# Performance work log

Measured on AMD Instinct MI355X. Metric: run time of the kernel, lower is better.

Reference implementation:

```python
import jax, jax.numpy as jnp
import numpy as np

N_NODES = 50000
N_EDGES = 800000
NEG_SLOPE = 0.2  # PyG GATConv default


def _gat_layer(x, src, dst, n, W, a_src, a_dst, b, concat):
    """One GATConv layer (PyG semantics, eval mode so attention dropout is off).

    x: [N, F_in], src/dst: [E'] (self loops included), W: [F_in, H*C],
    a_src/a_dst: [H, C], b: [H*C] if concat else [C].
    """
    H, C = a_src.shape
    h = (x @ W).reshape(n, H, C)                      # [N, H, C]
    al_s = jnp.sum(h * a_src, axis=-1)                # [N, H]
    al_d = jnp.sum(h * a_dst, axis=-1)                # [N, H]
    e = jax.nn.leaky_relu(al_s[src] + al_d[dst], NEG_SLOPE)  # [E', H]
    # numerically stable softmax over incoming edges of each dst node
    m = jax.lax.stop_gradient(jax.ops.segment_max(e, dst, num_segments=n))
    m = jnp.where(jnp.isfinite(m), m, 0.0)
    ex = jnp.exp(e - m[dst])                          # [E', H]
    denom = jax.ops.segment_sum(ex, dst, num_segments=n)     # [N, H]
    alpha = ex / denom[dst]                           # safe: self loops => denom > 0
    out = jax.ops.segment_sum(alpha[:, :, None] * h[src], dst, num_segments=n)  # [N,H,C]
    out = out.reshape(n, H * C) if concat else out.mean(axis=1)
    return out + b


def setup_inputs() -> dict:
    key = jax.random.key(0)
    ks = jax.random.split(key, 8)
    in_dim, hid, heads, out_dim = 256, 32, 8, 16
    x = jax.random.normal(ks[0], (N_NODES, in_dim), dtype=jnp.float32)
    edge_index = jax.random.randint(ks[1], (2, N_EDGES), 0, N_NODES, dtype=jnp.int64)
    s1 = 1.0 / np.sqrt(in_dim)
    s2 = 1.0 / np.sqrt(heads * hid)
    return {
        "x": x,
        "edge_index": edge_index,
        "W1": jax.random.normal(ks[2], (in_dim, heads * hid), dtype=jnp.float32) * s1,
        "a_src1": jax.random.normal(ks[3], (heads, hid), dtype=jnp.float32) * s2,
        "a_dst1": jax.random.normal(ks[4], (heads, hid), dtype=jnp.float32) * s2,
        "b1": jnp.zeros((heads * hid,), dtype=jnp.float32),
        "W2": jax.random.normal(ks[5], (heads * hid, out_dim), dtype=jnp.float32) * s2,
        "a_src2": jax.random.normal(ks[6], (1, out_dim), dtype=jnp.float32) * 0.25,
        "a_dst2": jax.random.normal(ks[7], (1, out_dim), dtype=jnp.float32) * 0.25,
        "b2": jnp.zeros((out_dim,), dtype=jnp.float32),
    }


def reference(x, edge_index, W1, a_src1, a_dst1, b1, W2, a_src2, a_dst2, b2):
    n = x.shape[0]
    loops = jnp.arange(n, dtype=edge_index.dtype)
    src = jnp.concatenate([edge_index[0], loops])  # add_self_loops (PyG default)
    dst = jnp.concatenate([edge_index[1], loops])
    h = jax.nn.relu(_gat_layer(x, src, dst, n, W1, a_src1, a_dst1, b1, concat=True))
    # F.dropout(p=0.5, training=False) -> identity in eval mode
    h = _gat_layer(h, src, dst, n, W2, a_src2, a_dst2, b2, concat=False)
    return jax.nn.log_softmax(h, axis=1)
```

## Files before the change

kernel.cpp:

```cpp
#include <hip/hip_runtime.h>
#include <hip/hip_bf16.h>


#define LRELU(x) ((x) > 0.f ? (x) : 0.2f * (x))

typedef __attribute__((ext_vector_type(8))) short short8;
typedef __attribute__((ext_vector_type(8))) unsigned short ushort8;
typedef __attribute__((ext_vector_type(4))) float f32x4;

__device__ inline unsigned short f2b(float f) {
    __hip_bfloat16 h = __float2bfloat16(f);
    return *reinterpret_cast<unsigned short*>(&h);
}
__device__ inline float b2f(unsigned short u) {
    __hip_bfloat16 h;
    *reinterpret_cast<unsigned short*>(&h) = u;
    return __bfloat162float(h);
}


__global__ void k_init_deg(int* deg, int n) {
    int i = blockIdx.x * blockDim.x + threadIdx.x;
    if (i < n) deg[i] = 1;
}

__global__ void k_hist(const int* __restrict__ dst, int* deg, int E) {
    int i = blockIdx.x * blockDim.x + threadIdx.x;
    if (i < E) atomicAdd(&deg[dst[i]], 1);
}


__global__ __launch_bounds__(256) void k_scanA(const int* __restrict__ deg,
                                               int* __restrict__ tmp,
                                               int* __restrict__ blocksum, int n) {
    __shared__ int sc[256];
    int b = blockIdx.x, t = threadIdx.x;
    int i = b * 256 + t;
    int v = (i < n) ? deg[i] : 0;
    sc[t] = v;
    __syncthreads();
    for (int off = 1; off < 256; off <<= 1) {
        int x = 0;
        if (t >= off) x = sc[t - off];
        __syncthreads();
        sc[t] += x;
        __syncthreads();
    }
    if (i < n) tmp[i] = sc[t] - v;
    if (t == 255) blocksum[b] = sc[255];
}

__global__ __launch_bounds__(256) void k_scanB(const int* __restrict__ blocksum,
                                               int* __restrict__ blockpre, int nb) {
    __shared__ int sc[256];
    int t = threadIdx.x;
    int v = (t < nb) ? blocksum[t] : 0;
    sc[t] = v;
    __syncthreads();
    for (int off = 1; off < 256; off <<= 1) {
        int x = 0;
        if (t >= off) x = sc[t - off];
        __syncthreads();
        sc[t] += x;
        __syncthreads();
    }
    if (t < nb) blockpre[t] = sc[t] - v;
}

__global__ __launch_bounds__(256) void k_scanC(const int* __restrict__ tmp,
                                               const int* __restrict__ blockpre,
                                               int* __restrict__ offs,
                                               int* __restrict__ cursor, int n, int P) {
    int b = blockIdx.x, t = threadIdx.x;
    int i = b * 256 + t;
    if (i < n) {
        int o = tmp[i] + blockpre[b];
        offs[i] = o;
        cursor[i] = o;
    }
    if (i == 0) offs[n] = P;
}

__global__ void k_scatter(const int* __restrict__ src, const int* __restrict__ dst,
                          int* cursor, int* __restrict__ csr, int* __restrict__ dstv,
                          int E, int n) {
    int i = blockIdx.x * blockDim.x + threadIdx.x;
    int s, d;
    if (i < E) {
        s = src[i];
        d = dst[i];
    } else if (i < E + n) {
        s = i - E;
        d = s;
    } else {
        return;
    }
    int p = atomicAdd(&cursor[d], 1);
    csr[p] = s;
    dstv[p] = d;
}


__global__ __launch_bounds__(256) void k_prepw(const float* __restrict__ W,
                                               unsigned short* __restrict__ Wt) {
    int k = blockIdx.x;
    int nn = threadIdx.x;
    Wt[nn * 256 + k] = f2b(W[k * 256 + nn]);
}


__global__ __launch_bounds__(256) void k_gemm1(const float* __restrict__ A,
                                               const unsigned short* __restrict__ Wt,
                                               unsigned short* __restrict__ h1b, int M) {
    __shared__ unsigned short As[128][40];
    __shared__ unsigned short Bs[128][40];
    int t = threadIdx.x;
    int r0 = blockIdx.x * 128, c0 = blockIdx.y * 128;
    int srow = t >> 1, shalf = t & 1;
    int lane = t & 63, w = t >> 6;
    int lane15 = lane & 15, quad = lane >> 4;
    int rbw = (w & 1) * 64, cbw = (w >> 1) * 64;

    f32x4 acc[4][4];
#pragma unroll
    for (int i = 0; i < 4; i++)
#pragma unroll
        for (int j = 0; j < 4; j++) acc[i][j] = (f32x4)0.f;

    for (int k0 = 0; k0 < 256; k0 += 32) {
        {
            int row = r0 + srow;
            ushort8 p0, p1;
            if (row < M) {
                const float4* sp = (const float4*)&A[(size_t)row * 256 + k0 + shalf * 16];
                float4 f0 = sp[0], f1 = sp[1], f2 = sp[2], f3 = sp[3];
                p0[0] = f2b(f0.x); p0[1] = f2b(f0.y); p0[2] = f2b(f0.z); p0[3] = f2b(f0.w);
                p0[4] = f2b(f1.x); p0[5] = f2b(f1.y); p0[6] = f2b(f1.z); p0[7] = f2b(f1.w);
                p1[0] = f2b(f2.x); p1[1] = f2b(f2.y); p1[2] = f2b(f2.z); p1[3] = f2b(f2.w);
                p1[4] = f2b(f3.x); p1[5] = f2b(f3.y); p1[6] = f2b(f3.z); p1[7] = f2b(f3.w);
            } else {
                p0 = (ushort8)0; p1 = (ushort8)0;
            }
            *(ushort8*)&As[srow][shalf * 16] = p0;
            *(ushort8*)&As[srow][shalf * 16 + 8] = p1;
            const ushort8* bp = (const ushort8*)&Wt[(size_t)(c0 + srow) * 256 + k0 + shalf * 16];
            *(ushort8*)&Bs[srow][shalf * 16] = bp[0];
            *(ushort8*)&Bs[srow][shalf * 16 + 8] = bp[1];
        }
        __syncthreads();
        short8 af[4], bf[4];
#pragma unroll
        for (int i = 0; i < 4; i++)
            af[i] = *(const short8*)&As[rbw + i * 16 + lane15][quad * 8];
#pragma unroll
        for (int j = 0; j < 4; j++)
            bf[j] = *(const short8*)&Bs[cbw + j * 16 + lane15][quad * 8];
#pragma unroll
        for (int i = 0; i < 4; i++)
#pragma unroll
            for (int j = 0; j < 4; j++)
                acc[i][j] = __builtin_amdgcn_mfma_f32_16x16x32_bf16(af[i], bf[j], acc[i][j], 0, 0, 0);
        __syncthreads();
    }
#pragma unroll
    for (int i = 0; i < 4; i++) {
        int rowb = r0 + rbw + i * 16 + quad * 4;
#pragma unroll
        for (int j = 0; j < 4; j++) {
            int col = c0 + cbw + j * 16 + lane15;
#pragma unroll
            for (int r = 0; r < 4; r++) {
                int row = rowb + r;
                if (row < M) h1b[(size_t)row * 256 + col] = f2b(acc[i][j][r]);
            }
        }
    }
}


__global__ __launch_bounds__(256) void k_al1(const unsigned short* __restrict__ h1b,
                                             const float* __restrict__ asrc,
                                             const float* __restrict__ adst,
                                             float* __restrict__ als,
                                             float* __restrict__ ald) {
    int v = blockIdx.x, t = threadIdx.x;
    float hv = b2f(h1b[(size_t)v * 256 + t]);
    float ps = hv * asrc[t], pd = hv * adst[t];
#pragma unroll
    for (int off = 16; off; off >>= 1) {
        ps += __shfl_down(ps, off, 32);
        pd += __shfl_down(pd, off, 32);
    }
    if ((t & 31) == 0) {
        int h = t >> 5;
        als[v * 8 + h] = ps;
        ald[v * 8 + h] = pd;
    }
}


__global__ void k_w1(const int* __restrict__ csr, const int* __restrict__ dstv,
                     const float* __restrict__ als, const float* __restrict__ ald,
                     float* __restrict__ w, int P) {
    int i = blockIdx.x * blockDim.x + threadIdx.x;
    if (i >= P * 8) return;
    int p = i >> 3, h = i & 7;
    int u = csr[p], d = dstv[p];
    float x = als[u * 8 + h] + ald[d * 8 + h];
    w[i] = __expf(LRELU(x));
}

__global__ void k_w2(const int* __restrict__ csr, const int* __restrict__ dstv,
                     const float* __restrict__ als, const float* __restrict__ ald,
                     float* __restrict__ w, int P) {
    int p = blockIdx.x * blockDim.x + threadIdx.x;
    if (p >= P) return;
    float x = als[csr[p]] + ald[dstv[p]];
    w[p] = __expf(LRELU(x));
}


__global__ __launch_bounds__(128) void k_agg1(const int* __restrict__ csr,
                                              const int* __restrict__ offs,
                                              const float* __restrict__ w1,
                                              const unsigned short* __restrict__ h1b,
                                              const float* __restrict__ b1,
                                              unsigned short* __restrict__ x2b) {
    int v = blockIdx.x;
    int t = threadIdx.x;
    int start = offs[v];
    int deg = offs[v + 1] - start;
    __shared__ int su[32];
    __shared__ float ws[256];
    int h = t >> 4;
    float a0 = 0.f, a1 = 0.f, wsum = 0.f;
    for (int base = 0; base < deg; base += 32) {
        int cnt = min(32, deg - base);
        if (base) __syncthreads();
        if (t < cnt) su[t] = csr[start + base + t];
        for (int i = t; i < cnt * 8; i += 128) ws[i] = w1[(size_t)(start + base) * 8 + i];
        __syncthreads();
        for (int e = 0; e < cnt; e++) {
            float wv = ws[e * 8 + h];
            const unsigned int* hp = (const unsigned int*)(h1b + (size_t)su[e] * 256);
            unsigned int pk = hp[t];
            float f0 = b2f((unsigned short)(pk & 0xffffu));
            float f1 = b2f((unsigned short)(pk >> 16));
            a0 += wv * f0;
            a1 += wv * f1;
            wsum += wv;
        }
    }
    const float2* b1v = (const float2*)b1;
    float2 bb = b1v[t];
    float inv = 1.0f / wsum;
    float o0 = a0 * inv + bb.x;
    float o1 = a1 * inv + bb.y;
    o0 = o0 > 0.f ? o0 : 0.f;
    o1 = o1 > 0.f ? o1 : 0.f;
    unsigned int opk = (unsigned int)f2b(o0) | ((unsigned int)f2b(o1) << 16);
    ((unsigned int*)(x2b + (size_t)v * 256))[t] = opk;
}


__global__ __launch_bounds__(256) void k_gemm2(const unsigned short* __restrict__ Xb,
                                               const float* __restrict__ W,
                                               const float* __restrict__ asrc,
                                               const float* __restrict__ adst,
                                               float* __restrict__ h2,
                                               float* __restrict__ als,
                                               float* __restrict__ ald, int n) {
    __shared__ float xs[16][260];
    __shared__ float ws[256 * 16];
    int t = threadIdx.x;
    int r0 = blockIdx.x * 16;
#pragma unroll
    for (int i = 0; i < 16; i++) ws[t + i * 256] = W[t + i * 256];
#pragma unroll
    for (int i = 0; i < 16; i++) {
        int row = r0 + i;
        xs[i][t] = (row < n) ? b2f(Xb[(size_t)row * 256 + t]) : 0.f;
    }
    __syncthreads();
    int nl = t >> 4, j = t & 15;
    float acc = 0.f;
    const float4* xv = (const float4*)&xs[nl][0];
#pragma unroll 8
    for (int k4 = 0; k4 < 64; k4++) {
        float4 a = xv[k4];
        int k = k4 * 4;
        acc += a.x * ws[k * 16 + j] + a.y * ws[(k + 1) * 16 + j] +
               a.z * ws[(k + 2) * 16 + j] + a.w * ws[(k + 3) * 16 + j];
    }
    int row = r0 + nl;
    float ps = acc * asrc[j], pd = acc * adst[j];
#pragma unroll
    for (int off = 8; off; off >>= 1) {
        ps += __shfl_down(ps, off, 16);
        pd += __shfl_down(pd, off, 16);
    }
    if (row < n) {
        h2[row * 16 + j] = acc;
        if (j == 0) {
            als[row] = ps;
            ald[row] = pd;
        }
    }
}


__global__ __launch_bounds__(256) void k_agg2(const int* __restrict__ csr,
                                              const int* __restrict__ offs,
                                              const float* __restrict__ w2,
                                              const float* __restrict__ h2,
                                              const float* __restrict__ b2,
                                              float* __restrict__ out, int n) {
    int v = blockIdx.x * 4 + (threadIdx.x >> 6);
    if (v >= n) return;
    int lane = threadIdx.x & 63;
    int start = offs[v];
    int deg = offs[v + 1] - start;
    int c = lane & 15, q = lane >> 4;
    float acc = 0.f, wsum = 0.f;
    for (int e = q; e < deg; e += 4) {
        int p = start + e;
        float wv = w2[p];
        int u = csr[p];
        acc += wv * h2[(size_t)u * 16 + c];
        wsum += wv;
    }
    acc += __shfl_xor(acc, 32, 64);
    acc += __shfl_xor(acc, 16, 64);
    wsum += __shfl_xor(wsum, 32, 64);
    wsum += __shfl_xor(wsum, 16, 64);
    float o = acc / wsum + b2[c];
    float mx = o;
#pragma unroll
    for (int off = 8; off; off >>= 1) mx = fmaxf(mx, __shfl_xor(mx, off, 16));
    float s = __expf(o - mx);
#pragma unroll
    for (int off = 8; off; off >>= 1) s += __shfl_xor(s, off, 16);
    float res = o - mx - __logf(s);
    if (q == 0) out[(size_t)v * 16 + c] = res;
}


extern "C" void kernel_launch(void* const* d_in, const int* in_sizes, int n_in,
                              void* d_out, int out_size, void* d_ws, size_t ws_size,
                              hipStream_t stream) {
    const float* x = (const float*)d_in[0];
    const int* ei = (const int*)d_in[1];
    const float* W1 = (const float*)d_in[2];
    const float* asrc1 = (const float*)d_in[3];
    const float* adst1 = (const float*)d_in[4];
    const float* b1 = (const float*)d_in[5];
    const float* W2 = (const float*)d_in[6];
    const float* asrc2 = (const float*)d_in[7];
    const float* adst2 = (const float*)d_in[8];
    const float* b2 = (const float*)d_in[9];
    float* out = (float*)d_out;

    int n = in_sizes[0] / 256;
    int E = in_sizes[1] / 2;
    int P = E + n;
    const int* src = ei;
    const int* dst = ei + E;
    int NB = (n + 255) / 256;

    char* p = (char*)d_ws;
    auto alloc = [&](size_t bytes) {
        void* r = (void*)p;
        p += (bytes + 255) & ~(size_t)255;
        return r;
    };
    unsigned short* h1b = (unsigned short*)alloc((size_t)n * 256 * 2);
    unsigned short* x2b = (unsigned short*)alloc((size_t)n * 256 * 2);
    unsigned short* W1t = (unsigned short*)alloc((size_t)256 * 256 * 2);
    float* als1 = (float*)alloc((size_t)n * 8 * 4);
    float* ald1 = (float*)alloc((size_t)n * 8 * 4);
    float* h2 = (float*)alloc((size_t)n * 16 * 4);
    float* als2 = (float*)alloc((size_t)n * 4);
    float* ald2 = (float*)alloc((size_t)n * 4);
    int* deg = (int*)alloc((size_t)n * 4);
    int* offs = (int*)alloc((size_t)(n + 1) * 4);
    int* cursor = (int*)alloc((size_t)n * 4);
    int* stmp = (int*)alloc((size_t)n * 4);
    int* blocksum = (int*)alloc((size_t)NB * 4);
    int* blockpre = (int*)alloc((size_t)NB * 4);
    int* csr = (int*)alloc((size_t)P * 4);
    int* dstv = (int*)alloc((size_t)P * 4);
    float* w1 = (float*)alloc((size_t)P * 8 * 4);
    float* w2 = (float*)alloc((size_t)P * 4);

    k_init_deg<<<(n + 255) / 256, 256, 0, stream>>>(deg, n);
    k_hist<<<(E + 255) / 256, 256, 0, stream>>>(dst, deg, E);
    k_scanA<<<NB, 256, 0, stream>>>(deg, stmp, blocksum, n);
    k_scanB<<<1, 256, 0, stream>>>(blocksum, blockpre, NB);
    k_scanC<<<NB, 256, 0, stream>>>(stmp, blockpre, offs, cursor, n, P);
    k_scatter<<<(P + 255) / 256, 256, 0, stream>>>(src, dst, cursor, csr, dstv, E, n);

    k_prepw<<<256, 256, 0, stream>>>(W1, W1t);
    k_gemm1<<<dim3((n + 127) / 128, 2), 256, 0, stream>>>(x, W1t, h1b, n);
    k_al1<<<n, 256, 0, stream>>>(h1b, asrc1, adst1, als1, ald1);
    k_w1<<<(P * 8 + 255) / 256, 256, 0, stream>>>(csr, dstv, als1, ald1, w1, P);
    k_agg1<<<n, 128, 0, stream>>>(csr, offs, w1, h1b, b1, x2b);

    k_gemm2<<<(n + 15) / 16, 256, 0, stream>>>(x2b, W2, asrc2, adst2, h2, als2, ald2, n);
    k_w2<<<(P + 255) / 256, 256, 0, stream>>>(csr, dstv, als2, ald2, w2, P);
    k_agg2<<<(n + 3) / 4, 256, 0, stream>>>(csr, offs, w2, h2, b2, out, n);
}
```

Before: 394.8 us.

## Fuse edge attention weights into aggregation kernels and drop dstv/w buffers

Removes the separate k_w1/k_w2 kernels and the per-edge weight and destination arrays. The exp(leaky_relu(als[u]+ald[v])) weights are now computed inside k_agg1 and k_agg2, and each block already knows its destination node. k_al1 is also restructured to handle four nodes per block, using vectorized loads and bit-shift bf16 decode. This saves two launches and the write and read of a 13 MB weight buffer. In exchange, exps are computed inside the aggregation loop and some threads sit idle there.

```diff
diff --git a/kernel.cpp b/kernel.cpp
--- a/kernel.cpp
+++ b/kernel.cpp
@@ -28,7 +28,6 @@
     int i = blockIdx.x * blockDim.x + threadIdx.x;
     if (i < E) atomicAdd(&deg[dst[i]], 1);
 }
-
 
 __global__ __launch_bounds__(256) void k_scanA(const int* __restrict__ deg,
                                                int* __restrict__ tmp,
@@ -82,8 +81,7 @@
 }
 
 __global__ void k_scatter(const int* __restrict__ src, const int* __restrict__ dst,
-                          int* cursor, int* __restrict__ csr, int* __restrict__ dstv,
-                          int E, int n) {
+                          int* cursor, int* __restrict__ csr, int E, int n) {
     int i = blockIdx.x * blockDim.x + threadIdx.x;
     int s, d;
     if (i < E) {
@@ -97,7 +95,6 @@
     }
     int p = atomicAdd(&cursor[d], 1);
     csr[p] = s;
-    dstv[p] = d;
 }
 
 
@@ -182,47 +179,37 @@
                                              const float* __restrict__ asrc,
                                              const float* __restrict__ adst,
                                              float* __restrict__ als,
-                                             float* __restrict__ ald) {
-    int v = blockIdx.x, t = threadIdx.x;
-    float hv = b2f(h1b[(size_t)v * 256 + t]);
-    float ps = hv * asrc[t], pd = hv * adst[t];
-#pragma unroll
-    for (int off = 16; off; off >>= 1) {
-        ps += __shfl_down(ps, off, 32);
-        pd += __shfl_down(pd, off, 32);
-    }
-    if ((t & 31) == 0) {
-        int h = t >> 5;
+                                             float* __restrict__ ald, int n) {
+    int v = blockIdx.x * 4 + (threadIdx.x >> 6);
+    if (v >= n) return;
+    int lane = threadIdx.x & 63;
+    const uint2* hp = (const uint2*)(h1b + (size_t)v * 256);
+    uint2 pk = hp[lane];
+    float f0 = __uint_as_float(pk.x << 16);
+    float f1 = __uint_as_float(pk.x & 0xffff0000u);
+    float f2 = __uint_as_float(pk.y << 16);
+    float f3 = __uint_as_float(pk.y & 0xffff0000u);
+    float4 a_s = ((const float4*)asrc)[lane];
+    float4 a_d = ((const float4*)adst)[lane];
+    float ps = f0 * a_s.x + f1 * a_s.y + f2 * a_s.z + f3 * a_s.w;
+    float pd = f0 * a_d.x + f1 * a_d.y + f2 * a_d.z + f3 * a_d.w;
+#pragma unroll
+    for (int off = 1; off < 8; off <<= 1) {
+        ps += __shfl_xor(ps, off, 64);
+        pd += __shfl_xor(pd, off, 64);
+    }
+    if ((lane & 7) == 0) {
+        int h = lane >> 3;
         als[v * 8 + h] = ps;
         ald[v * 8 + h] = pd;
     }
 }
 
 
-__global__ void k_w1(const int* __restrict__ csr, const int* __restrict__ dstv,
-                     const float* __restrict__ als, const float* __restrict__ ald,
-                     float* __restrict__ w, int P) {
-    int i = blockIdx.x * blockDim.x + threadIdx.x;
-    if (i >= P * 8) return;
-    int p = i >> 3, h = i & 7;
-    int u = csr[p], d = dstv[p];
-    float x = als[u * 8 + h] + ald[d * 8 + h];
-    w[i] = __expf(LRELU(x));
-}
-
-__global__ void k_w2(const int* __restrict__ csr, const int* __restrict__ dstv,
-                     const float* __restrict__ als, const float* __restrict__ ald,
-                     float* __restrict__ w, int P) {
-    int p = blockIdx.x * blockDim.x + threadIdx.x;
-    if (p >= P) return;
-    float x = als[csr[p]] + ald[dstv[p]];
-    w[p] = __expf(LRELU(x));
-}
-
-
 __global__ __launch_bounds__(128) void k_agg1(const int* __restrict__ csr,
                                               const int* __restrict__ offs,
-                                              const float* __restrict__ w1,
+                                              const float* __restrict__ als,
+                                              const float* __restrict__ aldg,
                                               const unsigned short* __restrict__ h1b,
                                               const float* __restrict__ b1,
                                               unsigned short* __restrict__ x2b) {
@@ -230,22 +217,41 @@
     int t = threadIdx.x;
     int start = offs[v];
     int deg = offs[v + 1] - start;
+    __shared__ float aldv[8];
     __shared__ int su[32];
     __shared__ float ws[256];
+    if (t < 8) aldv[t] = aldg[v * 8 + t];
+    __syncthreads();
     int h = t >> 4;
     float a0 = 0.f, a1 = 0.f, wsum = 0.f;
     for (int base = 0; base < deg; base += 32) {
         int cnt = min(32, deg - base);
         if (base) __syncthreads();
-        if (t < cnt) su[t] = csr[start + base + t];
-        for (int i = t; i < cnt * 8; i += 128) ws[i] = w1[(size_t)(start + base) * 8 + i];
+        if (t < cnt) {
+            int u = csr[start + base + t];
+            su[t] = u;
+            const float4* ap = (const float4*)(als + (size_t)u * 8);
+            float4 x0 = ap[0], x1 = ap[1];
+            float e0 = x0.x + aldv[0], e1 = x0.y + aldv[1];
+            float e2 = x0.z + aldv[2], e3 = x0.w + aldv[3];
+            float e4 = x1.x + aldv[4], e5 = x1.y + aldv[5];
+            float e6 = x1.z + aldv[6], e7 = x1.w + aldv[7];
+            ws[t * 8 + 0] = __expf(LRELU(e0));
+            ws[t * 8 + 1] = __expf(LRELU(e1));
+            ws[t * 8 + 2] = __expf(LRELU(e2));
+            ws[t * 8 + 3] = __expf(LRELU(e3));
+            ws[t * 8 + 4] = __expf(LRELU(e4));
+            ws[t * 8 + 5] = __expf(LRELU(e5));
+            ws[t * 8 + 6] = __expf(LRELU(e6));
+            ws[t * 8 + 7] = __expf(LRELU(e7));
+        }
         __syncthreads();
         for (int e = 0; e < cnt; e++) {
             float wv = ws[e * 8 + h];
             const unsigned int* hp = (const unsigned int*)(h1b + (size_t)su[e] * 256);
             unsigned int pk = hp[t];
-            float f0 = b2f((unsigned short)(pk & 0xffffu));
-            float f1 = b2f((unsigned short)(pk >> 16));
+            float f0 = __uint_as_float(pk << 16);
+            float f1 = __uint_as_float(pk & 0xffff0000u);
             a0 += wv * f0;
             a1 += wv * f1;
             wsum += wv;
@@ -311,7 +317,8 @@
 
 __global__ __launch_bounds__(256) void k_agg2(const int* __restrict__ csr,
                                               const int* __restrict__ offs,
-                                              const float* __restrict__ w2,
+                                              const float* __restrict__ als,
+                                              const float* __restrict__ aldg,
                                               const float* __restrict__ h2,
                                               const float* __restrict__ b2,
                                               float* __restrict__ out, int n) {
@@ -320,12 +327,13 @@
     int lane = threadIdx.x & 63;
     int start = offs[v];
     int deg = offs[v + 1] - start;
+    float aldv = aldg[v];
     int c = lane & 15, q = lane >> 4;
     float acc = 0.f, wsum = 0.f;
     for (int e = q; e < deg; e += 4) {
-        int p = start + e;
-        float wv = w2[p];
-        int u = csr[p];
+        int u = csr[start + e];
+        float x = als[u] + aldv;
+        float wv = __expf(LRELU(x));
         acc += wv * h2[(size_t)u * 16 + c];
         wsum += wv;
     }
@@ -388,24 +396,19 @@
     int* blocksum = (int*)alloc((size_t)NB * 4);
     int* blockpre = (int*)alloc((size_t)NB * 4);
     int* csr = (int*)alloc((size_t)P * 4);
-    int* dstv = (int*)alloc((size_t)P * 4);
-    float* w1 = (float*)alloc((size_t)P * 8 * 4);
-    float* w2 = (float*)alloc((size_t)P * 4);
 
     k_init_deg<<<(n + 255) / 256, 256, 0, stream>>>(deg, n);
     k_hist<<<(E + 255) / 256, 256, 0, stream>>>(dst, deg, E);
     k_scanA<<<NB, 256, 0, stream>>>(deg, stmp, blocksum, n);
     k_scanB<<<1, 256, 0, stream>>>(blocksum, blockpre, NB);
     k_scanC<<<NB, 256, 0, stream>>>(stmp, blockpre, offs, cursor, n, P);
-    k_scatter<<<(P + 255) / 256, 256, 0, stream>>>(src, dst, cursor, csr, dstv, E, n);
+    k_scatter<<<(P + 255) / 256, 256, 0, stream>>>(src, dst, cursor, csr, E, n);
 
     k_prepw<<<256, 256, 0, stream>>>(W1, W1t);
     k_gemm1<<<dim3((n + 127) / 128, 2), 256, 0, stream>>>(x, W1t, h1b, n);
-    k_al1<<<n, 256, 0, stream>>>(h1b, asrc1, adst1, als1, ald1);
-    k_w1<<<(P * 8 + 255) / 256, 256, 0, stream>>>(csr, dstv, als1, ald1, w1, P);
-    k_agg1<<<n, 128, 0, stream>>>(csr, offs, w1, h1b, b1, x2b);
+    k_al1<<<(n + 3) / 4, 256, 0, stream>>>(h1b, asrc1, adst1, als1, ald1, n);
+    k_agg1<<<n, 128, 0, stream>>>(csr, offs, als1, ald1, h1b, b1, x2b);
 
     k_gemm2<<<(n + 15) / 16, 256, 0, stream>>>(x2b, W2, asrc2, adst2, h2, als2, ald2, n);
-    k_w2<<<(P + 255) / 256, 256, 0, stream>>>(csr, dstv, als2, ald2, w2, P);
-    k_agg2<<<(n + 3) / 4, 256, 0, stream>>>(csr, offs, w2, h2, b2, out, n);
-}
+    k_agg2<<<(n + 3) / 4, 256, 0, stream>>>(csr, offs, als2, ald2, h2, b2, out, n);
+}
```

New measurement: 368.3 us. 6.7% less time.
